# Kernel tuning notes

Measured on AMD Instinct MI355X. Metric: run time of the kernel, lower is better.

Reference implementation:

```python
import jax, jax.numpy as jnp
import numpy as np

NEG_SLOPE = 0.2  # PyG GATConv default negative_slope


def _gat_dense(x, W, att_src, att_dst, bias):
    """PyG GATConv on a fully-connected graph (self-loops included) == dense attention.
    x: [N, F_in], W: [F_in, H*C], att_src/att_dst: [H, C], bias: [H*C] or [C].
    Returns per-head outputs [N, H, C] (bias added by caller after concat/mean).
    """
    H, C = att_src.shape
    N = x.shape[0]
    h = (x @ W).reshape(N, H, C)                      # transformed node feats
    s = jnp.einsum('nhc,hc->nh', h, att_src)          # alpha_src per source node
    t = jnp.einsum('nhc,hc->nh', h, att_dst)          # alpha_dst per dest node
    # e[i, j, h] = leaky_relu(alpha_dst[i] + alpha_src[j]); softmax over sources j
    e = jax.nn.leaky_relu(t[:, None, :] + s[None, :, :], NEG_SLOPE)  # [N, N, H]
    a = jax.nn.softmax(e, axis=1)
    out = jnp.einsum('ijh,jhc->ihc', a, h)            # aggregate sources -> dest
    return out


def setup_inputs() -> dict:
    key = jax.random.key(0)
    ks = jax.random.split(key, 11)
    N, D, C, H = 4096, 768, 128, 4
    sd1 = 1.0 / np.sqrt(D)
    sd2 = 1.0 / np.sqrt(H * C)
    sd3 = 1.0 / np.sqrt(C)
    return {
        'node_feats': jax.random.normal(ks[0], (N, D), dtype=jnp.float32),
        'W1': jax.random.normal(ks[1], (D, H * C), dtype=jnp.float32) * sd1,
        'att_src1': jax.random.normal(ks[2], (H, C), dtype=jnp.float32) * sd3,
        'att_dst1': jax.random.normal(ks[3], (H, C), dtype=jnp.float32) * sd3,
        'b1': jnp.zeros((H * C,), dtype=jnp.float32),
        'W2': jax.random.normal(ks[4], (H * C, C), dtype=jnp.float32) * sd2,
        'att_src2': jax.random.normal(ks[5], (1, C), dtype=jnp.float32) * sd3,
        'att_dst2': jax.random.normal(ks[6], (1, C), dtype=jnp.float32) * sd3,
        'b2': jnp.zeros((C,), dtype=jnp.float32),
        'fcW': jax.random.normal(ks[7], (C, D), dtype=jnp.float32) * sd3,
        'fcb': jnp.zeros((D,), dtype=jnp.float32),
    }


def reference(node_feats, W1, att_src1, att_dst1, b1, W2, att_src2, att_dst2, b2, fcW, fcb):
    N = node_feats.shape[0]
    # GAT layer 1: 4 heads, concat=True
    x = _gat_dense(node_feats, W1, att_src1, att_dst1, b1).reshape(N, -1) + b1
    x = jax.nn.elu(x)
    # GAT layer 2: 1 head, concat=False (mean over the single head == identity)
    x = _gat_dense(x, W2, att_src2, att_dst2, b2)[:, 0, :] + b2
    x = jax.nn.elu(x)
    x = x.mean(axis=0)            # [gat_hidden]
    return x @ fcW + fcb          # [hidden_dim]
```

## Files before the change

kernel.cpp:

```cpp
#include <hip/hip_runtime.h>
#include <hip/hip_bf16.h>


#define NNODE 4096
#define CDIM 128
#define TW 132
#define NEG 0.2f
#define CHUNK 64
#define NCHUNK 64

typedef __bf16 bf16x8 __attribute__((ext_vector_type(8)));
typedef float f32x4 __attribute__((ext_vector_type(4)));

__device__ __forceinline__ unsigned short f2b(float f) {
  unsigned int u = __float_as_uint(f);
  u += 0x7fffu + ((u >> 16) & 1u);
  return (unsigned short)(u >> 16);
}

__global__ __launch_bounds__(256) void prep_kernel(const float* __restrict__ x,
                                                   const float* __restrict__ W1,
                                                   const float* __restrict__ W2,
                                                   unsigned short* __restrict__ xb,
                                                   unsigned short* __restrict__ W1t,
                                                   unsigned short* __restrict__ W2t,
                                                   float* __restrict__ zs1,
                                                   float* __restrict__ zs2) {
  __shared__ float tile[64][65];
  int b = blockIdx.x, t = threadIdx.x;
  if (b < 3072) {
    int i = b * 256 + t;
    float4 v = ((const float4*)x)[i];
    ushort4 o;
    o.x = f2b(v.x); o.y = f2b(v.y); o.z = f2b(v.z); o.w = f2b(v.w);
    ((ushort4*)xb)[i] = o;
    return;
  }
  if (b >= 3184) {
    float4 z = {0.f, 0.f, 0.f, 0.f};
    if (b < 3216) {
      ((float4*)zs1)[(b - 3184) * 256 + t] = z;
    } else {
      ((float4*)zs2)[(b - 3216) * 256 + t] = z;
    }
    return;
  }
  const float* W; unsigned short* Wt; int K, N, n0, k0;
  if (b < 3072 + 96) {
    int b2 = b - 3072; W = W1; Wt = W1t; K = 768; N = 512;
    n0 = (b2 & 7) * 64; k0 = (b2 >> 3) * 64;
  } else {
    int b3 = b - 3072 - 96; W = W2; Wt = W2t; K = 512; N = 128;
    n0 = (b3 & 1) * 64; k0 = (b3 >> 1) * 64;
  }
  for (int p = 0; p < 16; p++) {
    int e = p * 256 + t;
    int rr = e >> 6, cc = e & 63;
    tile[rr][cc] = W[(size_t)(k0 + rr) * N + n0 + cc];
  }
  __syncthreads();
  for (int p = 0; p < 16; p++) {
    int e = p * 256 + t;
    int rr = e >> 6, cc = e & 63;
    Wt[(size_t)(n0 + rr) * K + k0 + cc] = f2b(tile[cc][rr]);
  }
}

template <int BM, int BN>
__global__ __launch_bounds__(256) void mfma_gemm_bt(const unsigned short* __restrict__ A,
                                                    const unsigned short* __restrict__ Bt,
                                                    float* __restrict__ C,
                                                    int M, int N, int K,
                                                    float* __restrict__ sAcc,
                                                    float* __restrict__ tAcc,
                                                    const float* __restrict__ av_s,
                                                    const float* __restrict__ av_d) {
  __shared__ __align__(16) unsigned short As[BM * 40];
  __shared__ __align__(16) unsigned short Bs[BN * 40];
  constexpr int WM = BM / 2, WN = BN / 2;
  constexpr int FI = WM / 16, FJ = WN / 16;
  constexpr int EA = BM * 32 / 8;
  constexpr int EB = BN * 32 / 8;
  constexpr int NA = (EA + 255) / 256;
  constexpr int NB = (EB + 255) / 256;
  int tid = threadIdx.x;
  int lane = tid & 63, wave = tid >> 6;
  int wm = (wave >> 1) * WM, wn = (wave & 1) * WN;
  int m0 = blockIdx.y * BM, n0 = blockIdx.x * BN;
  int fm = lane & 15, fq = lane >> 4;
  f32x4 acc[FI][FJ] = {};
  uint4 ar[NA], br[NB];
#pragma unroll
  for (int q = 0; q < NA; q++) {
    int e = q * 256 + tid;
    if (e < EA) {
      int r = e >> 2, kk = (e & 3) * 8;
      ar[q] = *(const uint4*)(A + (size_t)(m0 + r) * K + kk);
    }
  }
#pragma unroll
  for (int q = 0; q < NB; q++) {
    int e = q * 256 + tid;
    if (e < EB) {
      int r = e >> 2, kk = (e & 3) * 8;
      br[q] = *(const uint4*)(Bt + (size_t)(n0 + r) * K + kk);
    }
  }
  for (int k0 = 0; k0 < K; k0 += 32) {
    __syncthreads();
#pragma unroll
    for (int q = 0; q < NA; q++) {
      int e = q * 256 + tid;
      if (e < EA) {
        int r = e >> 2, kk = (e & 3) * 8;
        *(uint4*)&As[r * 40 + kk] = ar[q];
      }
    }
#pragma unroll
    for (int q = 0; q < NB; q++) {
      int e = q * 256 + tid;
      if (e < EB) {
        int r = e >> 2, kk = (e & 3) * 8;
        *(uint4*)&Bs[r * 40 + kk] = br[q];
      }
    }
    __syncthreads();
    if (k0 + 32 < K) {
#pragma unroll
      for (int q = 0; q < NA; q++) {
        int e = q * 256 + tid;
        if (e < EA) {
          int r = e >> 2, kk = (e & 3) * 8;
          ar[q] = *(const uint4*)(A + (size_t)(m0 + r) * K + k0 + 32 + kk);
        }
      }
#pragma unroll
      for (int q = 0; q < NB; q++) {
        int e = q * 256 + tid;
        if (e < EB) {
          int r = e >> 2, kk = (e & 3) * 8;
          br[q] = *(const uint4*)(Bt + (size_t)(n0 + r) * K + k0 + 32 + kk);
        }
      }
    }
    bf16x8 af[FI], bfr[FJ];
#pragma unroll
    for (int i = 0; i < FI; i++)
      af[i] = *(const bf16x8*)&As[(wm + i * 16 + fm) * 40 + fq * 8];
#pragma unroll
    for (int j = 0; j < FJ; j++)
      bfr[j] = *(const bf16x8*)&Bs[(wn + j * 16 + fm) * 40 + fq * 8];
#pragma unroll
    for (int i = 0; i < FI; i++)
#pragma unroll
      for (int j = 0; j < FJ; j++)
        acc[i][j] = __builtin_amdgcn_mfma_f32_16x16x32_bf16(af[i], bfr[j], acc[i][j], 0, 0, 0);
  }
#pragma unroll
  for (int i = 0; i < FI; i++) {
#pragma unroll
    for (int j = 0; j < FJ; j++) {
      int r = m0 + wm + i * 16 + fq * 4;
      int ccol = n0 + wn + j * 16 + fm;
#pragma unroll
      for (int reg = 0; reg < 4; reg++)
        C[(size_t)(r + reg) * N + ccol] = acc[i][j][reg];
    }
  }
  {
    int hh = n0 >> 7;
    float avs[FJ], avd[FJ];
#pragma unroll
    for (int j = 0; j < FJ; j++) {
      int col = n0 + wn + j * 16 + fm;
      avs[j] = av_s[col];
      avd[j] = av_d[col];
    }
#pragma unroll
    for (int i = 0; i < FI; i++) {
#pragma unroll
      for (int reg = 0; reg < 4; reg++) {
        float sv = 0.f, tv = 0.f;
#pragma unroll
        for (int j = 0; j < FJ; j++) {
          sv = fmaf(acc[i][j][reg], avs[j], sv);
          tv = fmaf(acc[i][j][reg], avd[j], tv);
        }
#pragma unroll
        for (int o = 1; o < 16; o <<= 1) {
          sv += __shfl_xor(sv, o, 64);
          tv += __shfl_xor(tv, o, 64);
        }
        if (fm == 0) {
          int row = m0 + wm + i * 16 + fq * 4 + reg;
          atomicAdd(&sAcc[(size_t)hh * NNODE + row], sv);
          atomicAdd(&tAcc[(size_t)hh * NNODE + row], tv);
        }
      }
    }
  }
}

__global__ __launch_bounds__(256) void rank_sort_kernel(const float* __restrict__ s,
                                                        float* __restrict__ ss,
                                                        int* __restrict__ si) {
  __shared__ __align__(16) float keys[NNODE];
  __shared__ int pc[8][32];
  int hh = blockIdx.y, tid = threadIdx.x;
  const float* sp = s + (size_t)hh * NNODE;
  for (int k = tid; k < NNODE / 4; k += 256)
    ((float4*)keys)[k] = ((const float4*)sp)[k];
  __syncthreads();
  int slot = tid & 31, part = tid >> 5;
  int node = blockIdx.x * 32 + slot;
  float mk = keys[node];
  int cnt = 0;
  int j0 = part * 512;
#pragma unroll 4
  for (int j = j0; j < j0 + 512; j += 4) {
    float4 kv = *(const float4*)&keys[j];
    cnt += (kv.x < mk) || (kv.x == mk && (j + 0) < node);
    cnt += (kv.y < mk) || (kv.y == mk && (j + 1) < node);
    cnt += (kv.z < mk) || (kv.z == mk && (j + 2) < node);
    cnt += (kv.w < mk) || (kv.w == mk && (j + 3) < node);
  }
  pc[part][slot] = cnt;
  __syncthreads();
  if (tid < 32) {
    int rank = 0;
#pragma unroll
    for (int p = 0; p < 8; p++) rank += pc[p][tid];
    int n2 = blockIdx.x * 32 + tid;
    ss[(size_t)hh * NNODE + rank] = keys[n2];
    si[(size_t)hh * NNODE + rank] = n2;
  }
}

__global__ __launch_bounds__(128) void passA_kernel(const float* __restrict__ h,
                                                    const float* __restrict__ ss,
                                                    const int* __restrict__ si,
                                                    float* __restrict__ partP,
                                                    float* __restrict__ partM, int H) {
  __shared__ float eP[CHUNK], eM[CHUNK];
  __shared__ int ids[CHUNK];
  int b = blockIdx.x, hh = b / NCHUNK, ci = b % NCHUNK;
  int c = threadIdx.x;
  int HC = H * CDIM;
  int base = ci * CHUNK;
  if (c < CHUNK) {
    float sv = ss[(size_t)hh * NNODE + base + c];
    ids[c] = si[(size_t)hh * NNODE + base + c];
    eP[c] = expf(sv);
    eM[c] = expf(NEG * sv);
  }
  __syncthreads();
  float sp = 0.f, sm = 0.f;
  for (int kb = 0; kb < CHUNK; kb += 8) {
    float v[8];
#pragma unroll
    for (int j = 0; j < 8; j++)
      v[j] = h[(size_t)ids[kb + j] * HC + hh * CDIM + c];
#pragma unroll
    for (int j = 0; j < 8; j++) {
      sp = fmaf(eP[kb + j], v[j], sp);
      sm = fmaf(eM[kb + j], v[j], sm);
    }
  }
  size_t o = ((size_t)hh * NCHUNK + ci) * TW;
  partP[o + c] = sp;
  partM[o + c] = sm;
  if (c == 0) {
    float zp = 0.f, zm = 0.f;
#pragma unroll
    for (int k = 0; k < CHUNK; k++) { zp += eP[k]; zm += eM[k]; }
    partP[o + 128] = zp;
    partM[o + 128] = zm;
  }
}

__global__ __launch_bounds__(128) void passC_kernel(const float* __restrict__ h,
                                                    const float* __restrict__ ss,
                                                    const int* __restrict__ si,
                                                    const float* __restrict__ partP,
                                                    const float* __restrict__ partM,
                                                    float* __restrict__ SS,
                                                    float* __restrict__ PP, int H) {
  __shared__ float hrow[CHUNK][CDIM];
  __shared__ float eP[CHUNK], eM[CHUNK];
  __shared__ int ids[CHUNK];
  int b = blockIdx.x, hh = b / NCHUNK, ci = b % NCHUNK;
  int c = threadIdx.x;
  int HC = H * CDIM;
  int base = ci * CHUNK;
  size_t hb = (size_t)hh * (NNODE + 1);
  if (c < CHUNK) {
    float sv = ss[(size_t)hh * NNODE + base + c];
    ids[c] = si[(size_t)hh * NNODE + base + c];
    eP[c] = expf(sv);
    eM[c] = expf(NEG * sv);
  }
  __syncthreads();
  float cm = 0.f, cp = 0.f;
  for (int g0 = 0; g0 < NCHUNK; g0 += 16) {
    float vm[16], vp[16];
#pragma unroll
    for (int j = 0; j < 16; j++) {
      size_t o = ((size_t)hh * NCHUNK + g0 + j) * TW + c;
      vm[j] = partM[o];
      vp[j] = partP[o];
    }
#pragma unroll
    for (int j = 0; j < 16; j++) {
      if (g0 + j < ci) cm += vm[j];
      if (g0 + j > ci) cp += vp[j];
    }
  }
  float zcm = 0.f, zcp = 0.f;
  if (c == 0) {
    for (int g0 = 0; g0 < NCHUNK; g0 += 16) {
      float vm[16], vp[16];
#pragma unroll
      for (int j = 0; j < 16; j++) {
        size_t o = ((size_t)hh * NCHUNK + g0 + j) * TW + 128;
        vm[j] = partM[o];
        vp[j] = partP[o];
      }
#pragma unroll
      for (int j = 0; j < 16; j++) {
        if (g0 + j < ci) zcm += vm[j];
        if (g0 + j > ci) zcp += vp[j];
      }
    }
  }
  for (int kb = 0; kb < CHUNK; kb += 8) {
    float v[8];
#pragma unroll
    for (int j = 0; j < 8; j++)
      v[j] = h[(size_t)ids[kb + j] * HC + hh * CDIM + c];
#pragma unroll
    for (int j = 0; j < 8; j++) hrow[kb + j][c] = v[j];
  }
  float runm = cm, runzm = zcm;
#pragma unroll 8
  for (int k = 0; k < CHUNK; k++) {
    size_t row = (hb + base + k) * TW;
    PP[row + c] = runm;
    if (c == 0) PP[row + 128] = runzm;
    runm = fmaf(eM[k], hrow[k][c], runm);
    runzm += eM[k];
  }
  if (ci == NCHUNK - 1) {
    size_t row = (hb + NNODE) * TW;
    PP[row + c] = runm;
    if (c == 0) PP[row + 128] = runzm;
  }
  float runp = cp, runzp = zcp;
#pragma unroll 8
  for (int k = CHUNK - 1; k >= 0; k--) {
    runp = fmaf(eP[k], hrow[k][c], runp);
    runzp += eP[k];
    size_t row = (hb + base + k) * TW;
    SS[row + c] = runp;
    if (c == 0) SS[row + 128] = runzp;
  }
  if (ci == NCHUNK - 1) {
    size_t row = (hb + NNODE) * TW;
    SS[row + c] = 0.f;
    if (c == 0) SS[row + 128] = 0.f;
  }
}

template <typename OUT>
__global__ __launch_bounds__(128) void attend_kernel(const float* __restrict__ SS,
                                                     const float* __restrict__ PP,
                                                     const float* __restrict__ ss,
                                                     const float* __restrict__ tt,
                                                     const float* __restrict__ bias,
                                                     OUT* __restrict__ out, int H) {
  int b = blockIdx.x;
  int n = b / H, hh = b % H;
  int c = threadIdx.x;
  float tv = tt[(size_t)hh * NNODE + n];
  const float* sp = ss + (size_t)hh * NNODE;
  float thr = -tv;
  int lo = 0, hi = NNODE;
  while (lo < hi) { int mid = (lo + hi) >> 1; if (sp[mid] < thr) lo = mid + 1; else hi = mid; }
  size_t hb = (size_t)hh * (NNODE + 1);
  float wp = expf(tv), wm = expf(NEG * tv);
  float num = wp * SS[(hb + lo) * TW + c] + wm * PP[(hb + lo) * TW + c];
  float Z = wp * SS[(hb + lo) * TW + 128] + wm * PP[(hb + lo) * TW + 128];
  float o = num / Z + bias[hh * CDIM + c];
  float r = (o > 0.f) ? o : (expf(o) - 1.f);
  if constexpr (sizeof(OUT) == 2)
    out[(size_t)n * (H * CDIM) + hh * CDIM + c] = f2b(r);
  else
    out[(size_t)n * (H * CDIM) + hh * CDIM + c] = r;
}

__global__ __launch_bounds__(256) void mean_part_kernel(const float* __restrict__ x,
                                                        float* __restrict__ part) {
  __shared__ float4 red[256];
  int b = blockIdx.x, tid = threadIdx.x;
  int q = tid & 31, r0 = tid >> 5;
  const float4* xp = (const float4*)x;
  float4 s = {0.f, 0.f, 0.f, 0.f};
  int base = b * 64;
  for (int r = r0; r < 64; r += 8) {
    float4 v = xp[(size_t)(base + r) * 32 + q];
    s.x += v.x; s.y += v.y; s.z += v.z; s.w += v.w;
  }
  red[tid] = s; __syncthreads();
  for (int off = 4; off > 0; off >>= 1) {
    if (r0 < off) {
      float4 o = red[tid + off * 32];
      red[tid].x += o.x; red[tid].y += o.y; red[tid].z += o.z; red[tid].w += o.w;
    }
    __syncthreads();
  }
  if (tid < 32) ((float4*)part)[b * 32 + tid] = red[tid];
}

__global__ __launch_bounds__(256) void fc_kernel(const float* __restrict__ part,
                                                 const float* __restrict__ fcW,
                                                 const float* __restrict__ fcb,
                                                 float* __restrict__ out) {
  __shared__ float tmp[256];
  __shared__ float m[CDIM];
  int tid = threadIdx.x;
  int c = tid & 127, half = tid >> 7;
  float a = 0.f;
  for (int g = half; g < 64; g += 2) a += part[g * CDIM + c];
  tmp[tid] = a; __syncthreads();
  if (tid < 128) m[tid] = (tmp[tid] + tmp[tid + 128]) * (1.f / NNODE);
  __syncthreads();
  int d = blockIdx.x * 256 + tid;
  float acc = fcb[d];
#pragma unroll 4
  for (int c2 = 0; c2 < CDIM; c2++) acc = fmaf(m[c2], fcW[c2 * 768 + d], acc);
  out[d] = acc;
}

extern "C" void kernel_launch(void* const* d_in, const int* in_sizes, int n_in,
                              void* d_out, int out_size, void* d_ws, size_t ws_size,
                              hipStream_t stream) {
  const float* x   = (const float*)d_in[0];
  const float* W1  = (const float*)d_in[1];
  const float* as1 = (const float*)d_in[2];
  const float* ad1 = (const float*)d_in[3];
  const float* b1  = (const float*)d_in[4];
  const float* W2  = (const float*)d_in[5];
  const float* as2 = (const float*)d_in[6];
  const float* ad2 = (const float*)d_in[7];
  const float* b2  = (const float*)d_in[8];
  const float* fcW = (const float*)d_in[9];
  const float* fcb = (const float*)d_in[10];

  float* ws = (float*)d_ws;
  size_t off = 0;
  auto alloc = [&](size_t nfloats) { float* p = ws + off; off += nfloats; return p; };

  float* h1  = alloc((size_t)NNODE * 512);
  float* x2f = alloc((size_t)NNODE * 256 + 64 + 16384);
  float* h2  = alloc((size_t)NNODE * 128);
  float* x3  = alloc((size_t)NNODE * 128);
  float* s1  = alloc((size_t)4 * NNODE);
  float* t1  = alloc((size_t)4 * NNODE);
  float* sS1 = alloc((size_t)4 * NNODE);
  int*   sI1 = (int*)alloc((size_t)4 * NNODE);
  float* SS1 = alloc((size_t)4 * (NNODE + 1) * TW);
  float* PP1 = alloc((size_t)4 * (NNODE + 1) * TW);
  float* pP1 = alloc((size_t)4 * NCHUNK * TW);
  float* pM1 = alloc((size_t)4 * NCHUNK * TW);
  float* s2  = alloc(NNODE);
  float* t2  = alloc(NNODE);
  float* sS2 = alloc(NNODE);
  int*   sI2 = (int*)alloc(NNODE);
  float* SS2 = alloc((size_t)(NNODE + 1) * TW);
  float* PP2 = alloc((size_t)(NNODE + 1) * TW);
  float* pP2 = alloc((size_t)NCHUNK * TW);
  float* pM2 = alloc((size_t)NCHUNK * TW);
  float* mpart = alloc((size_t)64 * CDIM);

  unsigned short* xb  = (unsigned short*)PP1;
  unsigned short* W1t = (unsigned short*)SS1;
  unsigned short* x2b = (unsigned short*)x2f;
  unsigned short* W2t = (unsigned short*)(x2f + NNODE * 256 + 64);

  prep_kernel<<<3224, 256, 0, stream>>>(x, W1, W2, xb, W1t, W2t, s1, s2);
  mfma_gemm_bt<64, 64><<<dim3(512 / 64, NNODE / 64), 256, 0, stream>>>(
      xb, W1t, h1, NNODE, 512, 768, s1, t1, as1, ad1);
  rank_sort_kernel<<<dim3(NNODE / 32, 4), 256, 0, stream>>>(s1, sS1, sI1);
  passA_kernel<<<4 * NCHUNK, 128, 0, stream>>>(h1, sS1, sI1, pP1, pM1, 4);
  passC_kernel<<<4 * NCHUNK, 128, 0, stream>>>(h1, sS1, sI1, pP1, pM1, SS1, PP1, 4);
  attend_kernel<unsigned short><<<NNODE * 4, 128, 0, stream>>>(SS1, PP1, sS1, t1, b1, x2b, 4);
  mfma_gemm_bt<32, 64><<<dim3(128 / 64, NNODE / 32), 256, 0, stream>>>(
      x2b, W2t, h2, NNODE, 128, 512, s2, t2, as2, ad2);
  rank_sort_kernel<<<dim3(NNODE / 32, 1), 256, 0, stream>>>(s2, sS2, sI2);
  passA_kernel<<<NCHUNK, 128, 0, stream>>>(h2, sS2, sI2, pP2, pM2, 1);
  passC_kernel<<<NCHUNK, 128, 0, stream>>>(h2, sS2, sI2, pP2, pM2, SS2, PP2, 1);
  attend_kernel<float><<<NNODE, 128, 0, stream>>>(SS2, PP2, sS2, t2, b2, x3, 1);
  mean_part_kernel<<<64, 256, 0, stream>>>(x3, mpart);
  fc_kernel<<<3, 256, 0, stream>>>(mpart, fcW, fcb, (float*)d_out);
}
```

Baseline: 225.0 us.

## Add chunk prefix-scan pass, precompute attend split indices in rank sort, halve chunk size

Adds a passB kernel that scans the per-chunk partial sums once into prefix and suffix arrays. passC now reads one value instead of looping over all chunks, which makes that cost linear rather than quadratic. The rank-sort kernel also counts, for each node, how many source keys fall below -t, so attend reads a precomputed split index instead of binary-searching global memory. CHUNK is halved to 32 (NCHUNK 128) to double block-level parallelism in passA and passC, at the cost of two more kernel launches and a serial per-head scan.

Result: faster. 209.6 us (-6.8%).

```diff
diff --git a/kernel.cpp b/kernel.cpp
--- a/kernel.cpp
+++ b/kernel.cpp
@@ -6,8 +6,8 @@
 #define CDIM 128
 #define TW 132
 #define NEG 0.2f
-#define CHUNK 64
-#define NCHUNK 64
+#define CHUNK 32
+#define NCHUNK 128
 
 typedef __bf16 bf16x8 __attribute__((ext_vector_type(8)));
 typedef float f32x4 __attribute__((ext_vector_type(4)));
@@ -202,10 +202,12 @@
 }
 
 __global__ __launch_bounds__(256) void rank_sort_kernel(const float* __restrict__ s,
+                                                        const float* __restrict__ t,
                                                         float* __restrict__ ss,
-                                                        int* __restrict__ si) {
+                                                        int* __restrict__ si,
+                                                        int* __restrict__ qlo) {
   __shared__ __align__(16) float keys[NNODE];
-  __shared__ int pc[8][32];
+  __shared__ int pc[8][32], qc[8][32];
   int hh = blockIdx.y, tid = threadIdx.x;
   const float* sp = s + (size_t)hh * NNODE;
   for (int k = tid; k < NNODE / 4; k += 256)
@@ -214,7 +216,8 @@
   int slot = tid & 31, part = tid >> 5;
   int node = blockIdx.x * 32 + slot;
   float mk = keys[node];
-  int cnt = 0;
+  float qk = -t[(size_t)hh * NNODE + node];
+  int cnt = 0, cq = 0;
   int j0 = part * 512;
 #pragma unroll 4
   for (int j = j0; j < j0 + 512; j += 4) {
@@ -223,8 +226,10 @@
     cnt += (kv.y < mk) || (kv.y == mk && (j + 1) < node);
     cnt += (kv.z < mk) || (kv.z == mk && (j + 2) < node);
     cnt += (kv.w < mk) || (kv.w == mk && (j + 3) < node);
+    cq += (kv.x < qk) + (kv.y < qk) + (kv.z < qk) + (kv.w < qk);
   }
   pc[part][slot] = cnt;
+  qc[part][slot] = cq;
   __syncthreads();
   if (tid < 32) {
     int rank = 0;
@@ -233,6 +238,12 @@
     int n2 = blockIdx.x * 32 + tid;
     ss[(size_t)hh * NNODE + rank] = keys[n2];
     si[(size_t)hh * NNODE + rank] = n2;
+  } else if (tid < 64) {
+    int sl = tid - 32;
+    int lo = 0;
+#pragma unroll
+    for (int p = 0; p < 8; p++) lo += qc[p][sl];
+    qlo[(size_t)hh * NNODE + blockIdx.x * 32 + sl] = lo;
   }
 }
 
@@ -278,11 +289,46 @@
   }
 }
 
+__global__ __launch_bounds__(192) void passB_kernel(const float* __restrict__ partP,
+                                                    const float* __restrict__ partM,
+                                                    float* __restrict__ sufP,
+                                                    float* __restrict__ prefM) {
+  int hh = blockIdx.y, dir = blockIdx.x;
+  int c = threadIdx.x;
+  if (c > 128) return;
+  size_t base = (size_t)hh * NCHUNK * TW;
+  if (dir == 0) {
+    float run = 0.f;
+    for (int g0 = 0; g0 < NCHUNK; g0 += 8) {
+      float v[8];
+#pragma unroll
+      for (int j = 0; j < 8; j++) v[j] = partM[base + (size_t)(g0 + j) * TW + c];
+#pragma unroll
+      for (int j = 0; j < 8; j++) {
+        prefM[base + (size_t)(g0 + j) * TW + c] = run;
+        run += v[j];
+      }
+    }
+  } else {
+    float run = 0.f;
+    for (int g0 = NCHUNK - 8; g0 >= 0; g0 -= 8) {
+      float v[8];
+#pragma unroll
+      for (int j = 7; j >= 0; j--) v[j] = partP[base + (size_t)(g0 + j) * TW + c];
+#pragma unroll
+      for (int j = 7; j >= 0; j--) {
+        sufP[base + (size_t)(g0 + j) * TW + c] = run;
+        run += v[j];
+      }
+    }
+  }
+}
+
 __global__ __launch_bounds__(128) void passC_kernel(const float* __restrict__ h,
                                                     const float* __restrict__ ss,
                                                     const int* __restrict__ si,
-                                                    const float* __restrict__ partP,
-                                                    const float* __restrict__ partM,
+                                                    const float* __restrict__ sufP,
+                                                    const float* __restrict__ prefM,
                                                     float* __restrict__ SS,
                                                     float* __restrict__ PP, int H) {
   __shared__ float hrow[CHUNK][CDIM];
@@ -300,38 +346,11 @@
     eM[c] = expf(NEG * sv);
   }
   __syncthreads();
-  float cm = 0.f, cp = 0.f;
-  for (int g0 = 0; g0 < NCHUNK; g0 += 16) {
-    float vm[16], vp[16];
-#pragma unroll
-    for (int j = 0; j < 16; j++) {
-      size_t o = ((size_t)hh * NCHUNK + g0 + j) * TW + c;
-      vm[j] = partM[o];
-      vp[j] = partP[o];
-    }
-#pragma unroll
-    for (int j = 0; j < 16; j++) {
-      if (g0 + j < ci) cm += vm[j];
-      if (g0 + j > ci) cp += vp[j];
-    }
-  }
+  size_t co = ((size_t)hh * NCHUNK + ci) * TW;
+  float cm = prefM[co + c];
+  float cp = sufP[co + c];
   float zcm = 0.f, zcp = 0.f;
-  if (c == 0) {
-    for (int g0 = 0; g0 < NCHUNK; g0 += 16) {
-      float vm[16], vp[16];
-#pragma unroll
-      for (int j = 0; j < 16; j++) {
-        size_t o = ((size_t)hh * NCHUNK + g0 + j) * TW + 128;
-        vm[j] = partM[o];
-        vp[j] = partP[o];
-      }
-#pragma unroll
-      for (int j = 0; j < 16; j++) {
-        if (g0 + j < ci) zcm += vm[j];
-        if (g0 + j > ci) zcp += vp[j];
-      }
-    }
-  }
+  if (c == 0) { zcm = prefM[co + 128]; zcp = sufP[co + 128]; }
   for (int kb = 0; kb < CHUNK; kb += 8) {
     float v[8];
 #pragma unroll
@@ -373,7 +392,7 @@
 template <typename OUT>
 __global__ __launch_bounds__(128) void attend_kernel(const float* __restrict__ SS,
                                                      const float* __restrict__ PP,
-                                                     const float* __restrict__ ss,
+                                                     const int* __restrict__ qlo,
                                                      const float* __restrict__ tt,
                                                      const float* __restrict__ bias,
                                                      OUT* __restrict__ out, int H) {
@@ -381,10 +400,7 @@
   int n = b / H, hh = b % H;
   int c = threadIdx.x;
   float tv = tt[(size_t)hh * NNODE + n];
-  const float* sp = ss + (size_t)hh * NNODE;
-  float thr = -tv;
-  int lo = 0, hi = NNODE;
-  while (lo < hi) { int mid = (lo + hi) >> 1; if (sp[mid] < thr) lo = mid + 1; else hi = mid; }
+  int lo = qlo[(size_t)hh * NNODE + n];
   size_t hb = (size_t)hh * (NNODE + 1);
   float wp = expf(tv), wm = expf(NEG * tv);
   float num = wp * SS[(hb + lo) * TW + c] + wm * PP[(hb + lo) * TW + c];
@@ -467,18 +483,24 @@
   float* t1  = alloc((size_t)4 * NNODE);
   float* sS1 = alloc((size_t)4 * NNODE);
   int*   sI1 = (int*)alloc((size_t)4 * NNODE);
+  int*   qL1 = (int*)alloc((size_t)4 * NNODE);
   float* SS1 = alloc((size_t)4 * (NNODE + 1) * TW);
   float* PP1 = alloc((size_t)4 * (NNODE + 1) * TW);
   float* pP1 = alloc((size_t)4 * NCHUNK * TW);
   float* pM1 = alloc((size_t)4 * NCHUNK * TW);
+  float* fP1 = alloc((size_t)4 * NCHUNK * TW);
+  float* fM1 = alloc((size_t)4 * NCHUNK * TW);
   float* s2  = alloc(NNODE);
   float* t2  = alloc(NNODE);
   float* sS2 = alloc(NNODE);
   int*   sI2 = (int*)alloc(NNODE);
+  int*   qL2 = (int*)alloc(NNODE);
   float* SS2 = alloc((size_t)(NNODE + 1) * TW);
   float* PP2 = alloc((size_t)(NNODE + 1) * TW);
   float* pP2 = alloc((size_t)NCHUNK * TW);
   float* pM2 = alloc((size_t)NCHUNK * TW);
+  float* fP2 = alloc((size_t)NCHUNK * TW);
+  float* fM2 = alloc((size_t)NCHUNK * TW);
   float* mpart = alloc((size_t)64 * CDIM);
 
   unsigned short* xb  = (unsigned short*)PP1;
@@ -489,16 +511,18 @@
   prep_kernel<<<3224, 256, 0, stream>>>(x, W1, W2, xb, W1t, W2t, s1, s2);
   mfma_gemm_bt<64, 64><<<dim3(512 / 64, NNODE / 64), 256, 0, stream>>>(
       xb, W1t, h1, NNODE, 512, 768, s1, t1, as1, ad1);
-  rank_sort_kernel<<<dim3(NNODE / 32, 4), 256, 0, stream>>>(s1, sS1, sI1);
+  rank_sort_kernel<<<dim3(NNODE / 32, 4), 256, 0, stream>>>(s1, t1, sS1, sI1, qL1);
   passA_kernel<<<4 * NCHUNK, 128, 0, stream>>>(h1, sS1, sI1, pP1, pM1, 4);
-  passC_kernel<<<4 * NCHUNK, 128, 0, stream>>>(h1, sS1, sI1, pP1, pM1, SS1, PP1, 4);
-  attend_kernel<unsigned short><<<NNODE * 4, 128, 0, stream>>>(SS1, PP1, sS1, t1, b1, x2b, 4);
+  passB_kernel<<<dim3(2, 4), 192, 0, stream>>>(pP1, pM1, fP1, fM1);
+  passC_kernel<<<4 * NCHUNK, 128, 0, stream>>>(h1, sS1, sI1, fP1, fM1, SS1, PP1, 4);
+  attend_kernel<unsigned short><<<NNODE * 4, 128, 0, stream>>>(SS1, PP1, qL1, t1, b1, x2b, 4);
   mfma_gemm_bt<32, 64><<<dim3(128 / 64, NNODE / 32), 256, 0, stream>>>(
       x2b, W2t, h2, NNODE, 128, 512, s2, t2, as2, ad2);
-  rank_sort_kernel<<<dim3(NNODE / 32, 1), 256, 0, stream>>>(s2, sS2, sI2);
+  rank_sort_kernel<<<dim3(NNODE / 32, 1), 256, 0, stream>>>(s2, t2, sS2, sI2, qL2);
   passA_kernel<<<NCHUNK, 128, 0, stream>>>(h2, sS2, sI2, pP2, pM2, 1);
-  passC_kernel<<<NCHUNK, 128, 0, stream>>>(h2, sS2, sI2, pP2, pM2, SS2, PP2, 1);
-  attend_kernel<float><<<NNODE, 128, 0, stream>>>(SS2, PP2, sS2, t2, b2, x3, 1);
+  passB_kernel<<<dim3(2, 1), 192, 0, stream>>>(pP2, pM2, fP2, fM2);
+  passC_kernel<<<NCHUNK, 128, 0, stream>>>(h2, sS2, sI2, fP2, fM2, SS2, PP2, 1);
+  attend_kernel<float><<<NNODE, 128, 0, stream>>>(SS2, PP2, qL2, t2, b2, x3, 1);
   mean_part_kernel<<<64, 256, 0, stream>>>(x3, mpart);
   fc_kernel<<<3, 256, 0, stream>>>(mpart, fcW, fcb, (float*)d_out);
 }
```
